# Performance work log

Measured on AMD Instinct MI355X. Metric: run time of the kernel, lower is better.

The kernel has to match this reference:

```python
import jax, jax.numpy as jnp
import numpy as np
import math

B, T, D, H = 256, 256, 128, 256  # batch, steps, input_size, hidden_size

def _uniform(k, shape, stdv):
    return jax.random.uniform(k, shape, jnp.float32, -stdv, stdv)

def setup_inputs() -> dict:
    key = jax.random.key(0)
    ks = jax.random.split(key, 16)
    X = jax.random.normal(ks[0], (B, T, D), jnp.float32)
    X_last_obsv = jax.random.normal(ks[1], (B, T, D), jnp.float32)
    Mask = (jax.random.uniform(ks[2], (B, T, D)) > 0.5).astype(jnp.float32)
    Delta = jax.random.uniform(ks[3], (B, T, D), jnp.float32) * 5.0
    X_mean = jax.random.normal(ks[4], (1, T, D), jnp.float32) * 0.1
    s_gate = 1.0 / math.sqrt(D + H + D)
    Wz = _uniform(ks[5], (H, D + H + D), s_gate); bz = _uniform(ks[6], (H,), s_gate)
    Wr = _uniform(ks[7], (H, D + H + D), s_gate); br = _uniform(ks[8], (H,), s_gate)
    Wh = _uniform(ks[9], (H, D + H + D), s_gate); bh = _uniform(ks[10], (H,), s_gate)
    s_x = 1.0 / math.sqrt(D)
    Wgx = _uniform(ks[11], (D, D), s_x); bgx = _uniform(ks[12], (D,), s_x)
    Wgh = _uniform(ks[13], (H, D), s_x); bgh = _uniform(ks[14], (H,), s_x)
    return {"X": X, "X_last_obsv": X_last_obsv, "Mask": Mask, "Delta": Delta,
            "X_mean": X_mean, "Wz": Wz, "bz": bz, "Wr": Wr, "br": br,
            "Wh": Wh, "bh": bh, "Wgx": Wgx, "bgx": bgx, "Wgh": Wgh, "bgh": bgh}

def reference(X, X_last_obsv, Mask, Delta, X_mean, Wz, bz, Wr, br, Wh, bh, Wgx, bgx, Wgh, bgh):
    # FilterLinear: weight masked by identity -> effectively a diagonal linear map
    Wgx_masked = jnp.eye(D, dtype=Wgx.dtype) * Wgx  # [D, D]

    def step(h, inp):
        x, xl, m, d, xm = inp  # x,xl,m,d: [B,D]; xm: [D]
        delta_x = jnp.exp(-jax.nn.relu(d @ Wgx_masked.T + bgx))  # [B,D]
        x = m * x + (1.0 - m) * (delta_x * xl + (1.0 - delta_x) * xm)
        delta_h = jnp.exp(-jax.nn.relu(d @ Wgh.T + bgh))          # [B,H]
        h = delta_h * h
        comb = jnp.concatenate([x, h, m], axis=1)                  # [B, D+H+D]
        z = jax.nn.sigmoid(comb @ Wz.T + bz)
        r = jax.nn.sigmoid(comb @ Wr.T + br)
        comb3 = jnp.concatenate([x, r * h, m], axis=1)
        h_tilde = jnp.tanh(comb3 @ Wh.T + bh)
        h = (1.0 - z) * h + z * h_tilde
        return h, h

    xs = (jnp.swapaxes(X, 0, 1), jnp.swapaxes(X_last_obsv, 0, 1),
          jnp.swapaxes(Mask, 0, 1), jnp.swapaxes(Delta, 0, 1), X_mean[0])  # [T,...]
    h0 = jnp.zeros((B, H), X.dtype)
    _, outs = jax.lax.scan(step, h0, xs)   # [T,B,H]
    outputs = jnp.swapaxes(outs, 0, 1)     # [B,T,H]
    return outputs, outputs[:, -1, :]
```

## Files before the change

kernel.cpp:

```cpp
#include <hip/hip_runtime.h>

#define B_ 256
#define T_ 256
#define D_ 128
#define H_ 256

typedef _Float16 f16;
typedef f16 f16x2 __attribute__((ext_vector_type(2)));
typedef short bf16x8 __attribute__((ext_vector_type(8)));
typedef float f32x4 __attribute__((ext_vector_type(4)));

__device__ __forceinline__ unsigned short f2bf(float f) {
  union { float f; unsigned u; } c; c.f = f;
  unsigned r = c.u + 0x7fffu + ((c.u >> 16) & 1u);
  return (unsigned short)(r >> 16);
}
__device__ __forceinline__ float bf2f(unsigned short s) {
  union { unsigned u; float f; } c; c.u = ((unsigned)s) << 16;
  return c.f;
}
__device__ __forceinline__ float dot2(f16x2 a, f16x2 b, float c) {
  return __builtin_amdgcn_fdot2(a, b, c, false);
}
__device__ __forceinline__ void gload16(const void* g, void* l) {
  __builtin_amdgcn_global_load_lds(
      (const __attribute__((address_space(1))) void*)g,
      (__attribute__((address_space(3))) void*)l, 16, 0, 0);
}

__global__ void prep_A(const float* __restrict__ X, const float* __restrict__ Xl,
                       const float* __restrict__ Mk, const float* __restrict__ Dl,
                       const float* __restrict__ Xm, const float* __restrict__ Wgx,
                       const float* __restrict__ bgx, unsigned short* __restrict__ A) {
  const int idx = blockIdx.x * 256 + threadIdx.x;
  const int i = idx >> 7;
  const int k = idx & 127;
  const int t = i & (T_ - 1);
  const float d = Dl[idx];
  const float m = Mk[idx];
  const float dx = __expf(-fmaxf(fmaf(d, Wgx[k * 129], bgx[k]), 0.f));
  const float xe = m * X[idx] + (1.f - m) * (dx * Xl[idx] + (1.f - dx) * Xm[t * 128 + k]);
  unsigned short* Ar = A + (size_t)i * 384;
  Ar[k]       = f2bf(xe);
  Ar[128 + k] = f2bf(m);
  Ar[256 + k] = f2bf(d);
}

__global__ void prep_B(const float* __restrict__ Wz, const float* __restrict__ bz,
                       const float* __restrict__ Wr, const float* __restrict__ br,
                       const float* __restrict__ Wh, const float* __restrict__ bh,
                       const float* __restrict__ Wgh, const float* __restrict__ bgh,
                       unsigned short* __restrict__ Bt, float* __restrict__ bias) {
  const int idx = blockIdx.x * 256 + threadIdx.x;
  if (idx >= 1024 * 384) return;
  const int j = idx / 384;
  const int k = idx - j * 384;
  float v = 0.f;
  if (j < 768) {
    const float* W = (j < 256) ? Wz : (j < 512) ? Wr : Wh;
    const int jj = j & 255;
    if (k < 128) v = W[jj * 512 + k];
    else if (k < 256) v = W[jj * 512 + 384 + (k - 128)];
  } else {
    if (k >= 256) v = Wgh[(j - 768) * 128 + (k - 256)];
  }
  Bt[idx] = f2bf(v);
  if (k == 0)
    bias[j] = (j < 256) ? bz[j] : (j < 512) ? br[j - 256] : (j < 768) ? bh[j - 512] : bgh[j - 768];
}

__global__ __launch_bounds__(256) void gemm_k(
    const unsigned short* __restrict__ A, const unsigned short* __restrict__ Bt,
    const float* __restrict__ bias, unsigned short* __restrict__ pre,
    f16* __restrict__ dhb, int jbase, int kstart, int kend) {
  __shared__ unsigned short As[128 * 64];
  __shared__ unsigned short Bs[128 * 64];
  const int tid = threadIdx.x;
  const int wave = tid >> 6;
  const int lane = tid & 63;
  const int i0 = blockIdx.y * 128;
  const int j0 = jbase + blockIdx.x * 128;
  const int wr = wave >> 1, wc = wave & 1;
  f32x4 acc[4][4] = {};
  for (int kb = kstart; kb < kend; kb += 64) {
    __syncthreads();
#pragma unroll
    for (int it = 0; it < 4; ++it) {
      const int r = wave * 32 + it * 8 + (lane >> 3);
      const int cb = (lane & 7) * 8;
      gload16(A  + (size_t)(i0 + r) * 384 + kb + cb, As + (wave * 32 + it * 8) * 64);
      gload16(Bt + (size_t)(j0 + r) * 384 + kb + cb, Bs + (wave * 32 + it * 8) * 64);
    }
    __syncthreads();
#pragma unroll
    for (int ks = 0; ks < 2; ++ks) {
      bf16x8 af[4], bfr[4];
#pragma unroll
      for (int m = 0; m < 4; ++m) {
        const int row = wr * 64 + m * 16 + (lane & 15);
        af[m] = *(const bf16x8*)(As + row * 64 + ks * 32 + (lane >> 4) * 8);
      }
#pragma unroll
      for (int n = 0; n < 4; ++n) {
        const int col = wc * 64 + n * 16 + (lane & 15);
        bfr[n] = *(const bf16x8*)(Bs + col * 64 + ks * 32 + (lane >> 4) * 8);
      }
#pragma unroll
      for (int m = 0; m < 4; ++m)
#pragma unroll
        for (int n = 0; n < 4; ++n)
          acc[m][n] = __builtin_amdgcn_mfma_f32_16x16x32_bf16(af[m], bfr[n], acc[m][n], 0, 0, 0);
    }
  }
#pragma unroll
  for (int m = 0; m < 4; ++m) {
    const int row0 = i0 + wr * 64 + m * 16 + ((lane >> 4) << 2);
#pragma unroll
    for (int n = 0; n < 4; ++n) {
      const int col = j0 + wc * 64 + n * 16 + (lane & 15);
      const float bv = bias[col];
#pragma unroll
      for (int q = 0; q < 4; ++q) {
        const float v = acc[m][n][q] + bv;
        const size_t r = (size_t)(row0 + q);
        if (jbase < 768) pre[r * 768 + col] = f2bf(v);
        else             dhb[r * 256 + (col - 768)] = (f16)__expf(-fmaxf(v, 0.f));
      }
    }
  }
}

__global__ __launch_bounds__(512, 2) void grud_seq(
    const float* __restrict__ Wz, const float* __restrict__ Wr, const float* __restrict__ Wh,
    const unsigned short* __restrict__ pre, const f16* __restrict__ dhb,
    float* __restrict__ out, float* __restrict__ out_last) {
  const int b = blockIdx.x;
  const int tid = threadIdx.x;
  const int j2 = tid & 255;
  const int khalf = tid >> 8;
  __shared__ __align__(16) f16 hh[H_];
  __shared__ __align__(16) f16 rhh[H_];
  __shared__ float scr[H_];

  f16x2 w1[128];
  {
    const float* Wg = (tid < 256) ? Wz : Wr;
#pragma unroll
    for (int kk = 0; kk < 128; ++kk) {
      float2 wv = *(const float2*)(Wg + j2 * 512 + 128 + kk * 2);
      w1[kk].x = (f16)wv.x; w1[kk].y = (f16)wv.y;
    }
  }
  f16x2 w2[64];
#pragma unroll
  for (int kk = 0; kk < 64; ++kk) {
    float2 wv = *(const float2*)(Wh + j2 * 512 + 128 + khalf * 128 + kk * 2);
    w2[kk].x = (f16)wv.x; w2[kk].y = (f16)wv.y;
  }

  float hreg = 0.f, zreg = 0.f, h1reg = 0.f;
  const size_t rowbase = (size_t)b * T_;
  float* outb = out + (size_t)b * T_ * H_;

  for (int t = 0; t < T_; ++t) {
    const size_t rowi = rowbase + t;
    const unsigned short* prow = pre + rowi * 768;
    if (tid < 256) {
      float dv = (float)dhb[rowi * 256 + tid];
      h1reg = dv * hreg;
      hh[tid] = (f16)h1reg;
    }
    __syncthreads();
    float g0 = 0, g1 = 0, g2 = 0, g3 = 0;
    {
      const uint4* hv = (const uint4*)hh;
#pragma unroll
      for (int q = 0; q < 32; ++q) {
        uint4 hw = hv[q];
        g0 = dot2(w1[4 * q + 0], __builtin_bit_cast(f16x2, hw.x), g0);
        g1 = dot2(w1[4 * q + 1], __builtin_bit_cast(f16x2, hw.y), g1);
        g2 = dot2(w1[4 * q + 2], __builtin_bit_cast(f16x2, hw.z), g2);
        g3 = dot2(w1[4 * q + 3], __builtin_bit_cast(f16x2, hw.w), g3);
      }
    }
    {
      float a = bf2f(prow[tid]) + ((g0 + g1) + (g2 + g3));
      float gate = 1.f / (1.f + __expf(-a));
      if (tid < 256) {
        zreg = gate;
      } else {
        float h1f = (float)hh[j2];
        rhh[j2] = (f16)(gate * h1f);
      }
    }
    __syncthreads();
    float c0 = 0, c1 = 0, c2 = 0, c3 = 0;
    {
      const uint4* rv = (const uint4*)rhh;
#pragma unroll
      for (int q = 0; q < 16; ++q) {
        uint4 rw = rv[khalf * 16 + q];
        c0 = dot2(w2[4 * q + 0], __builtin_bit_cast(f16x2, rw.x), c0);
        c1 = dot2(w2[4 * q + 1], __builtin_bit_cast(f16x2, rw.y), c1);
        c2 = dot2(w2[4 * q + 2], __builtin_bit_cast(f16x2, rw.z), c2);
        c3 = dot2(w2[4 * q + 3], __builtin_bit_cast(f16x2, rw.w), c3);
      }
    }
    float csum = (c0 + c1) + (c2 + c3);
    if (khalf) scr[j2] = csum;
    __syncthreads();
    if (tid < 256) {
      float tot = bf2f(prow[512 + tid]) + csum + scr[tid];
      float e = __expf(-2.f * tot);
      float htil = (1.f - e) / (1.f + e);
      float hn = (1.f - zreg) * h1reg + zreg * htil;
      outb[t * H_ + tid] = hn;
      hreg = hn;
    }
  }
  if (tid < 256) out_last[(size_t)b * H_ + tid] = hreg;
}

extern "C" void kernel_launch(void* const* d_in, const int* in_sizes, int n_in,
                              void* d_out, int out_size, void* d_ws, size_t ws_size,
                              hipStream_t stream) {
  const float* X   = (const float*)d_in[0];
  const float* Xl  = (const float*)d_in[1];
  const float* Mk  = (const float*)d_in[2];
  const float* Dl  = (const float*)d_in[3];
  const float* Xm  = (const float*)d_in[4];
  const float* Wz  = (const float*)d_in[5];
  const float* bz  = (const float*)d_in[6];
  const float* Wr  = (const float*)d_in[7];
  const float* br  = (const float*)d_in[8];
  const float* Wh  = (const float*)d_in[9];
  const float* bh  = (const float*)d_in[10];
  const float* Wgx = (const float*)d_in[11];
  const float* bgx = (const float*)d_in[12];
  const float* Wgh = (const float*)d_in[13];
  const float* bgh = (const float*)d_in[14];

  char* ws = (char*)d_ws;
  unsigned short* A    = (unsigned short*)(ws);
  unsigned short* Bt   = (unsigned short*)(ws + 50331648);
  float*          bias = (float*)(ws + 51118080);
  unsigned short* pre  = (unsigned short*)(ws + 51122176);
  f16*            dhb  = (f16*)(ws + 151785472);

  float* out = (float*)d_out;
  float* out_last = out + (size_t)B_ * T_ * H_;

  prep_A<<<dim3(32768), dim3(256), 0, stream>>>(X, Xl, Mk, Dl, Xm, Wgx, bgx, A);
  prep_B<<<dim3(1536), dim3(256), 0, stream>>>(Wz, bz, Wr, br, Wh, bh, Wgh, bgh, Bt, bias);
  gemm_k<<<dim3(6, 512), dim3(256), 0, stream>>>(A, Bt, bias, pre, dhb, 0, 0, 256);
  gemm_k<<<dim3(2, 512), dim3(256), 0, stream>>>(A, Bt, bias, pre, dhb, 768, 256, 384);
  grud_seq<<<dim3(256), dim3(512), 0, stream>>>(Wz, Wr, Wh, pre, dhb, out, out_last);
}
```

Baseline: 630.4 us.

## Split recurrent kernel across four lanes per hidden unit with shuffle reductions

The sequential GRU-D kernel now runs 1024 threads per batch row, with four lanes cooperating on each hidden unit. The gate and candidate dot products are split across lanes and combined with __shfl_xor instead of a shared-memory scratch array. Per-step precomputed inputs are prefetched one timestep ahead into registers. Per-thread weight registers are halved, allowing higher occupancy and a shorter serial dot-product chain, at the cost of an extra barrier per step and more threads contending at each barrier.

```diff
diff --git a/kernel.cpp b/kernel.cpp
--- a/kernel.cpp
+++ b/kernel.cpp
@@ -130,53 +130,73 @@
   }
 }
 
-__global__ __launch_bounds__(512, 2) void grud_seq(
+__global__ __launch_bounds__(1024, 4) void grud_seq(
     const float* __restrict__ Wz, const float* __restrict__ Wr, const float* __restrict__ Wh,
     const unsigned short* __restrict__ pre, const f16* __restrict__ dhb,
     float* __restrict__ out, float* __restrict__ out_last) {
   const int b = blockIdx.x;
   const int tid = threadIdx.x;
-  const int j2 = tid & 255;
-  const int khalf = tid >> 8;
+  const int j = tid >> 2;
+  const int sub = tid & 3;
+  const int gatebit = sub >> 1;
+  const int khalf = sub & 1;
+  const int kq = sub;
+  const bool owner = (sub == 0);
+  const bool rwriter = (sub == 2);
+
   __shared__ __align__(16) f16 hh[H_];
   __shared__ __align__(16) f16 rhh[H_];
-  __shared__ float scr[H_];
-
-  f16x2 w1[128];
+
+  f16x2 w1[64];
   {
-    const float* Wg = (tid < 256) ? Wz : Wr;
-#pragma unroll
-    for (int kk = 0; kk < 128; ++kk) {
-      float2 wv = *(const float2*)(Wg + j2 * 512 + 128 + kk * 2);
+    const float* Wg = gatebit ? Wr : Wz;
+    const float* src = Wg + j * 512 + 128 + khalf * 128;
+#pragma unroll
+    for (int kk = 0; kk < 64; ++kk) {
+      float2 wv = *(const float2*)(src + kk * 2);
       w1[kk].x = (f16)wv.x; w1[kk].y = (f16)wv.y;
     }
   }
-  f16x2 w2[64];
-#pragma unroll
-  for (int kk = 0; kk < 64; ++kk) {
-    float2 wv = *(const float2*)(Wh + j2 * 512 + 128 + khalf * 128 + kk * 2);
-    w2[kk].x = (f16)wv.x; w2[kk].y = (f16)wv.y;
+  f16x2 w2[32];
+  {
+    const float* src = Wh + j * 512 + 128 + kq * 64;
+#pragma unroll
+    for (int kk = 0; kk < 32; ++kk) {
+      float2 wv = *(const float2*)(src + kk * 2);
+      w2[kk].x = (f16)wv.x; w2[kk].y = (f16)wv.y;
+    }
   }
 
   float hreg = 0.f, zreg = 0.f, h1reg = 0.f;
-  const size_t rowbase = (size_t)b * T_;
-  float* outb = out + (size_t)b * T_ * H_;
+
+  unsigned idxB  = (unsigned)b * T_ * 768 + (unsigned)gatebit * 256 + j;
+  unsigned idxD  = (unsigned)b * T_ * 768 + 512 + j;
+  unsigned idxdh = (unsigned)b * T_ * 256 + j;
+  unsigned idxO  = (unsigned)b * T_ * 256 + j;
+
+  float pB_c = bf2f(pre[idxB]);
+  float dv_c = 0.f, pD_c = 0.f;
+  if (owner) { dv_c = (float)dhb[idxdh]; pD_c = bf2f(pre[idxD]); }
 
   for (int t = 0; t < T_; ++t) {
-    const size_t rowi = rowbase + t;
-    const unsigned short* prow = pre + rowi * 768;
-    if (tid < 256) {
-      float dv = (float)dhb[rowi * 256 + tid];
-      h1reg = dv * hreg;
-      hh[tid] = (f16)h1reg;
-    }
-    __syncthreads();
+    if (owner) {
+      h1reg = dv_c * hreg;
+      hh[j] = (f16)h1reg;
+    }
+    __syncthreads();
+
+    float pB_n = 0.f, dv_n = 0.f, pD_n = 0.f;
+    if (t + 1 < T_) {
+      pB_n = bf2f(pre[idxB + 768]);
+      if (owner) { dv_n = (float)dhb[idxdh + 256]; pD_n = bf2f(pre[idxD + 768]); }
+    }
+
     float g0 = 0, g1 = 0, g2 = 0, g3 = 0;
     {
       const uint4* hv = (const uint4*)hh;
 #pragma unroll
-      for (int q = 0; q < 32; ++q) {
-        uint4 hw = hv[q];
+      for (int q = 0; q < 16; ++q) {
+        uint4 hw = hv[khalf * 16 + q];
         g0 = dot2(w1[4 * q + 0], __builtin_bit_cast(f16x2, hw.x), g0);
         g1 = dot2(w1[4 * q + 1], __builtin_bit_cast(f16x2, hw.y), g1);
         g2 = dot2(w1[4 * q + 2], __builtin_bit_cast(f16x2, hw.z), g2);
@@ -184,22 +204,21 @@
       }
     }
     {
-      float a = bf2f(prow[tid]) + ((g0 + g1) + (g2 + g3));
+      float gs = (g0 + g1) + (g2 + g3);
+      gs += __shfl_xor(gs, 1);
+      float a = pB_c + gs;
       float gate = 1.f / (1.f + __expf(-a));
-      if (tid < 256) {
-        zreg = gate;
-      } else {
-        float h1f = (float)hh[j2];
-        rhh[j2] = (f16)(gate * h1f);
-      }
-    }
-    __syncthreads();
+      if (owner) zreg = gate;
+      if (rwriter) rhh[j] = (f16)(gate * (float)hh[j]);
+    }
+    __syncthreads();
+
     float c0 = 0, c1 = 0, c2 = 0, c3 = 0;
     {
       const uint4* rv = (const uint4*)rhh;
 #pragma unroll
-      for (int q = 0; q < 16; ++q) {
-        uint4 rw = rv[khalf * 16 + q];
+      for (int q = 0; q < 8; ++q) {
+        uint4 rw = rv[kq * 8 + q];
         c0 = dot2(w2[4 * q + 0], __builtin_bit_cast(f16x2, rw.x), c0);
         c1 = dot2(w2[4 * q + 1], __builtin_bit_cast(f16x2, rw.y), c1);
         c2 = dot2(w2[4 * q + 2], __builtin_bit_cast(f16x2, rw.z), c2);
@@ -207,18 +226,23 @@
       }
     }
     float csum = (c0 + c1) + (c2 + c3);
-    if (khalf) scr[j2] = csum;
-    __syncthreads();
-    if (tid < 256) {
-      float tot = bf2f(prow[512 + tid]) + csum + scr[tid];
+    csum += __shfl_xor(csum, 1);
+    csum += __shfl_xor(csum, 2);
+
+    if (owner) {
+      float tot = pD_c + csum;
       float e = __expf(-2.f * tot);
       float htil = (1.f - e) / (1.f + e);
       float hn = (1.f - zreg) * h1reg + zreg * htil;
-      outb[t * H_ + tid] = hn;
+      out[idxO] = hn;
       hreg = hn;
     }
-  }
-  if (tid < 256) out_last[(size_t)b * H_ + tid] = hreg;
+    __syncthreads();
+
+    idxB += 768; idxD += 768; idxdh += 256; idxO += 256;
+    pB_c = pB_n; dv_c = dv_n; pD_c = pD_n;
+  }
+  if (owner) out_last[(unsigned)b * H_ + j] = hreg;
 }
 
 extern "C" void kernel_launch(void* const* d_in, const int* in_sizes, int n_in,
@@ -254,5 +278,5 @@
   prep_B<<<dim3(1536), dim3(256), 0, stream>>>(Wz, bz, Wr, br, Wh, bh, Wgh, bgh, Bt, bias);
   gemm_k<<<dim3(6, 512), dim3(256), 0, stream>>>(A, Bt, bias, pre, dhb, 0, 0, 256);
   gemm_k<<<dim3(2, 512), dim3(256), 0, stream>>>(A, Bt, bias, pre, dhb, 768, 256, 384);
-  grud_seq<<<dim3(256), dim3(512), 0, stream>>>(Wz, Wr, Wh, pre, dhb, out, out_last);
-}
+  grud_seq<<<dim3(256), dim3(1024), 0, stream>>>(Wz, Wr, Wh, pre, dhb, out, out_last);
+}
```

After: 987.3 us. 56.6% more time.

## Run recurrence with one thread per hidden unit holding all three gate weight rows

Applied to the files above, without the earlier changes.

The sequential GRU kernel moves from 512 threads, split across gates and K-halves, to 256 threads where each thread keeps its full Wz, Wr and Wh rows in registers as packed fp16. This removes the third barrier and the scratch reduction for the candidate gate. The per-step precomputed gate inputs are prefetched one step ahead, which hides their global-load latency. In exchange each thread does twice the dot products, about 384 registers of weights, and runs at one wave per EU, so spilling or lower latency hiding are possible.

```diff
diff --git a/kernel.cpp b/kernel.cpp
--- a/kernel.cpp
+++ b/kernel.cpp
@@ -19,8 +19,14 @@
   union { unsigned u; float f; } c; c.u = ((unsigned)s) << 16;
   return c.f;
 }
-__device__ __forceinline__ float dot2(f16x2 a, f16x2 b, float c) {
-  return __builtin_amdgcn_fdot2(a, b, c, false);
+__device__ __forceinline__ float dot2u(unsigned w, unsigned h, float acc) {
+  return __builtin_amdgcn_fdot2(__builtin_bit_cast(f16x2, w),
+                                __builtin_bit_cast(f16x2, h), acc, false);
+}
+__device__ __forceinline__ unsigned packh2(float x, float y) {
+  unsigned short lo = __builtin_bit_cast(unsigned short, (f16)x);
+  unsigned short hi = __builtin_bit_cast(unsigned short, (f16)y);
+  return ((unsigned)hi << 16) | lo;
 }
 __device__ __forceinline__ void gload16(const void* g, void* l) {
   __builtin_amdgcn_global_load_lds(
@@ -130,95 +136,98 @@
   }
 }
 
-__global__ __launch_bounds__(512, 2) void grud_seq(
+__global__ __launch_bounds__(256)
+__attribute__((amdgpu_waves_per_eu(1, 1)))
+void grud_seq(
     const float* __restrict__ Wz, const float* __restrict__ Wr, const float* __restrict__ Wh,
     const unsigned short* __restrict__ pre, const f16* __restrict__ dhb,
     float* __restrict__ out, float* __restrict__ out_last) {
   const int b = blockIdx.x;
-  const int tid = threadIdx.x;
-  const int j2 = tid & 255;
-  const int khalf = tid >> 8;
+  const int j = threadIdx.x;
+
   __shared__ __align__(16) f16 hh[H_];
   __shared__ __align__(16) f16 rhh[H_];
-  __shared__ float scr[H_];
-
-  f16x2 w1[128];
+
+  unsigned wz[128], wr[128], wh[128];
   {
-    const float* Wg = (tid < 256) ? Wz : Wr;
-#pragma unroll
-    for (int kk = 0; kk < 128; ++kk) {
-      float2 wv = *(const float2*)(Wg + j2 * 512 + 128 + kk * 2);
-      w1[kk].x = (f16)wv.x; w1[kk].y = (f16)wv.y;
-    }
-  }
-  f16x2 w2[64];
-#pragma unroll
-  for (int kk = 0; kk < 64; ++kk) {
-    float2 wv = *(const float2*)(Wh + j2 * 512 + 128 + khalf * 128 + kk * 2);
-    w2[kk].x = (f16)wv.x; w2[kk].y = (f16)wv.y;
-  }
-
-  float hreg = 0.f, zreg = 0.f, h1reg = 0.f;
-  const size_t rowbase = (size_t)b * T_;
-  float* outb = out + (size_t)b * T_ * H_;
+    const float2* rz = (const float2*)(Wz + j * 512 + 128);
+    const float2* rrw = (const float2*)(Wr + j * 512 + 128);
+    const float2* rh = (const float2*)(Wh + j * 512 + 128);
+#pragma unroll
+    for (int p = 0; p < 128; ++p) { float2 a = rz[p];  wz[p] = packh2(a.x, a.y); }
+#pragma unroll
+    for (int p = 0; p < 128; ++p) { float2 a = rrw[p]; wr[p] = packh2(a.x, a.y); }
+#pragma unroll
+    for (int p = 0; p < 128; ++p) { float2 a = rh[p];  wh[p] = packh2(a.x, a.y); }
+  }
+
+  unsigned ip = (unsigned)b * T_ * 768 + j;
+  unsigned id = (unsigned)b * T_ * 256 + j;
+
+  float hreg = 0.f;
+  float pz_c = bf2f(pre[ip]);
+  float pr_c = bf2f(pre[ip + 256]);
+  float ph_c = bf2f(pre[ip + 512]);
+  float dv_c = (float)dhb[id];
 
   for (int t = 0; t < T_; ++t) {
-    const size_t rowi = rowbase + t;
-    const unsigned short* prow = pre + rowi * 768;
-    if (tid < 256) {
-      float dv = (float)dhb[rowi * 256 + tid];
-      h1reg = dv * hreg;
-      hh[tid] = (f16)h1reg;
-    }
-    __syncthreads();
-    float g0 = 0, g1 = 0, g2 = 0, g3 = 0;
+    float h1 = dv_c * hreg;
+    hh[j] = (f16)h1;
+    __syncthreads();
+
+    float pz_n = 0.f, pr_n = 0.f, ph_n = 0.f, dv_n = 0.f;
+    if (t + 1 < T_) {
+      pz_n = bf2f(pre[ip + 768]);
+      pr_n = bf2f(pre[ip + 768 + 256]);
+      ph_n = bf2f(pre[ip + 768 + 512]);
+      dv_n = (float)dhb[id + 256];
+    }
+
+    float az0 = 0, az1 = 0, az2 = 0, az3 = 0;
+    float ar0 = 0, ar1 = 0, ar2 = 0, ar3 = 0;
     {
       const uint4* hv = (const uint4*)hh;
 #pragma unroll
       for (int q = 0; q < 32; ++q) {
         uint4 hw = hv[q];
-        g0 = dot2(w1[4 * q + 0], __builtin_bit_cast(f16x2, hw.x), g0);
-        g1 = dot2(w1[4 * q + 1], __builtin_bit_cast(f16x2, hw.y), g1);
-        g2 = dot2(w1[4 * q + 2], __builtin_bit_cast(f16x2, hw.z), g2);
-        g3 = dot2(w1[4 * q + 3], __builtin_bit_cast(f16x2, hw.w), g3);
-      }
-    }
-    {
-      float a = bf2f(prow[tid]) + ((g0 + g1) + (g2 + g3));
-      float gate = 1.f / (1.f + __expf(-a));
-      if (tid < 256) {
-        zreg = gate;
-      } else {
-        float h1f = (float)hh[j2];
-        rhh[j2] = (f16)(gate * h1f);
-      }
-    }
-    __syncthreads();
+        az0 = dot2u(wz[4 * q + 0], hw.x, az0);
+        ar0 = dot2u(wr[4 * q + 0], hw.x, ar0);
+        az1 = dot2u(wz[4 * q + 1], hw.y, az1);
+        ar1 = dot2u(wr[4 * q + 1], hw.y, ar1);
+        az2 = dot2u(wz[4 * q + 2], hw.z, az2);
+        ar2 = dot2u(wr[4 * q + 2], hw.z, ar2);
+        az3 = dot2u(wz[4 * q + 3], hw.w, az3);
+        ar3 = dot2u(wr[4 * q + 3], hw.w, ar3);
+      }
+    }
+    float z = 1.f / (1.f + __expf(-(pz_c + ((az0 + az1) + (az2 + az3)))));
+    float r = 1.f / (1.f + __expf(-(pr_c + ((ar0 + ar1) + (ar2 + ar3)))));
+    rhh[j] = (f16)(r * h1);
+    __syncthreads();
+
     float c0 = 0, c1 = 0, c2 = 0, c3 = 0;
     {
       const uint4* rv = (const uint4*)rhh;
 #pragma unroll
-      for (int q = 0; q < 16; ++q) {
-        uint4 rw = rv[khalf * 16 + q];
-        c0 = dot2(w2[4 * q + 0], __builtin_bit_cast(f16x2, rw.x), c0);
-        c1 = dot2(w2[4 * q + 1], __builtin_bit_cast(f16x2, rw.y), c1);
-        c2 = dot2(w2[4 * q + 2], __builtin_bit_cast(f16x2, rw.z), c2);
-        c3 = dot2(w2[4 * q + 3], __builtin_bit_cast(f16x2, rw.w), c3);
-      }
-    }
-    float csum = (c0 + c1) + (c2 + c3);
-    if (khalf) scr[j2] = csum;
-    __syncthreads();
-    if (tid < 256) {
-      float tot = bf2f(prow[512 + tid]) + csum + scr[tid];
-      float e = __expf(-2.f * tot);
-      float htil = (1.f - e) / (1.f + e);
-      float hn = (1.f - zreg) * h1reg + zreg * htil;
-      outb[t * H_ + tid] = hn;
-      hreg = hn;
-    }
-  }
-  if (tid < 256) out_last[(size_t)b * H_ + tid] = hreg;
+      for (int q = 0; q < 32; ++q) {
+        uint4 rw = rv[q];
+        c0 = dot2u(wh[4 * q + 0], rw.x, c0);
+        c1 = dot2u(wh[4 * q + 1], rw.y, c1);
+        c2 = dot2u(wh[4 * q + 2], rw.z, c2);
+        c3 = dot2u(wh[4 * q + 3], rw.w, c3);
+      }
+    }
+    float tot = ph_c + ((c0 + c1) + (c2 + c3));
+    float e = __expf(-2.f * tot);
+    float htil = (1.f - e) / (1.f + e);
+    float hn = (1.f - z) * h1 + z * htil;
+    out[id] = hn;
+    hreg = hn;
+
+    ip += 768; id += 256;
+    pz_c = pz_n; pr_c = pr_n; ph_c = ph_n; dv_c = dv_n;
+  }
+  out_last[(unsigned)b * H_ + j] = hreg;
 }
 
 extern "C" void kernel_launch(void* const* d_in, const int* in_sizes, int n_in,
@@ -254,5 +263,5 @@
   prep_B<<<dim3(1536), dim3(256), 0, stream>>>(Wz, bz, Wr, br, Wh, bh, Wgh, bgh, Bt, bias);
   gemm_k<<<dim3(6, 512), dim3(256), 0, stream>>>(A, Bt, bias, pre, dhb, 0, 0, 256);
   gemm_k<<<dim3(2, 512), dim3(256), 0, stream>>>(A, Bt, bias, pre, dhb, 768, 256, 384);
-  grud_seq<<<dim3(256), dim3(512), 0, stream>>>(Wz, Wr, Wh, pre, dhb, out, out_last);
-}
+  grud_seq<<<dim3(256), dim3(256), 0, stream>>>(Wz, Wr, Wh, pre, dhb, out, out_last);
+}
```

After: 979.8 us. 1.55x slower.
